# Performance work log

Hardware: AMD Instinct MI355X
Metric: run time of the kernel (lower is better)

The kernel has to match this reference:

```python
import jax, jax.numpy as jnp
import numpy as np

EPS = 1e-6


def setup_inputs() -> dict:
    key = jax.random.key(0)
    k_x, k_w1, k_w2 = jax.random.split(key, 3)
    S, B, H, F = 2048, 4, 2048, 8192
    x = jax.random.normal(k_x, (S, B, H), dtype=jnp.float32)
    scale = jnp.ones((H,), dtype=jnp.float32)
    ln_bias = jnp.zeros((H,), dtype=jnp.float32)
    # kernel_1: [hidden, n_activations=2, intermediate] (GEGLU-style gated MLP)
    kernel_1 = jax.random.normal(k_w1, (H, 2, F), dtype=jnp.float32) * 0.02
    kernel_2 = jax.random.normal(k_w2, (F, H), dtype=jnp.float32) * 0.02
    return {"x": x, "scale": scale, "ln_bias": ln_bias,
            "kernel_1": kernel_1, "kernel_2": kernel_2}


def _layernorm(x, scale, bias):
    # fp32 layernorm over the last (hidden) axis, zero_centered_gamma=False
    mu = jnp.mean(x, axis=-1, keepdims=True)
    var = jnp.mean(jnp.square(x - mu), axis=-1, keepdims=True)
    y = (x - mu) * jax.lax.rsqrt(var + EPS)
    return y * scale + bias


def reference(x, scale, ln_bias, kernel_1, kernel_2):
    # x: [S, B, H] (transpose_batch_sequence=True layout)
    ln_out = _layernorm(x, scale, ln_bias)
    # First GEMM: one projection per activation slice -> [S, B, 2, F]
    z = jnp.einsum("sbh,haf->sbaf", ln_out, kernel_1)
    # activations = ('gelu', 'linear'): gated product
    act = jax.nn.gelu(z[..., 0, :], approximate=True) * z[..., 1, :]
    # Second GEMM: [S, B, F] @ [F, H] -> [S, B, H]
    out = jnp.einsum("sbf,fh->sbh", act, kernel_2)
    return out
```

## Files before the change

kernel.cpp:

```cpp
#include <hip/hip_runtime.h>
#include <hip/hip_bf16.h>

typedef short bf16x8 __attribute__((ext_vector_type(8)));
typedef float f32x4 __attribute__((ext_vector_type(4)));

__device__ inline short f2bf(float f) {
    __bf16 h = (__bf16)f;
    return __builtin_bit_cast(short, h);
}

__device__ inline void gload_lds16(const void* g, void* l) {
    __builtin_amdgcn_global_load_lds(
        (const __attribute__((address_space(1))) void*)g,
        (__attribute__((address_space(3))) void*)l, 16, 0, 0);
}

__global__ __launch_bounds__(256) void ln_kernel(const float* __restrict__ x,
                                                 const float* __restrict__ sc,
                                                 const float* __restrict__ bs,
                                                 short* __restrict__ o) {
    __shared__ float red[8];
    const int row = blockIdx.x;
    const int t = threadIdx.x;
    const float* xr = x + (size_t)row * 2048 + t * 8;
    float4 a = *(const float4*)xr;
    float4 b = *(const float4*)(xr + 4);
    float v[8] = {a.x, a.y, a.z, a.w, b.x, b.y, b.z, b.w};
    float s = 0.f, q = 0.f;
#pragma unroll
    for (int j = 0; j < 8; ++j) { s += v[j]; q += v[j] * v[j]; }
#pragma unroll
    for (int off = 32; off; off >>= 1) {
        s += __shfl_down(s, off, 64);
        q += __shfl_down(q, off, 64);
    }
    const int wv = t >> 6, ln = t & 63;
    if (ln == 0) { red[wv] = s; red[4 + wv] = q; }
    __syncthreads();
    s = red[0] + red[1] + red[2] + red[3];
    q = red[4] + red[5] + red[6] + red[7];
    const float mu = s * (1.f / 2048.f);
    const float var = q * (1.f / 2048.f) - mu * mu;
    const float rstd = rsqrtf(var + 1e-6f);
    const float* scp = sc + t * 8;
    const float* bp = bs + t * 8;
    bf16x8 ov;
#pragma unroll
    for (int j = 0; j < 8; ++j) ov[j] = f2bf((v[j] - mu) * rstd * scp[j] + bp[j]);
    *(bf16x8*)(o + (size_t)row * 2048 + t * 8) = ov;
}

__global__ __launch_bounds__(256) void transpose_conv(const float* __restrict__ src,
                                                      short* __restrict__ dst,
                                                      int R, int C) {
    __shared__ float tile[32][33];
    const int tc = blockIdx.x, tr = blockIdx.y;
    const int t = threadIdx.x;
    const int c = t & 31, r8 = t >> 5;
#pragma unroll
    for (int rr = r8; rr < 32; rr += 8)
        tile[rr][c] = src[(size_t)(tr * 32 + rr) * C + tc * 32 + c];
    __syncthreads();
#pragma unroll
    for (int rr = r8; rr < 32; rr += 8)
        dst[(size_t)(tc * 32 + rr) * R + tr * 32 + c] = f2bf(tile[c][rr]);
}

__global__ __launch_bounds__(256) void gemm1_geglu(const short* __restrict__ A,
                                                   const short* __restrict__ Bt,
                                                   short* __restrict__ act) {
    constexpr int K = 2048;
    constexpr int NACT = 8192;
    __shared__ short As[128 * 32];
    __shared__ short Bs[128 * 32];
    const int t = threadIdx.x;
    const int lane = t & 63;
    const int wv = t >> 6;
    const int wr = wv >> 1, wc = wv & 1;
    const int lr = lane & 15, lg = lane >> 4;
    const int m0 = blockIdx.y * 128;
    const int c0 = blockIdx.x * 64;

    const int srow = t >> 2;
    const int scol = (t & 3) * 8;
    const size_t a_b0 = (size_t)(m0 + srow) * K + scol;
    const size_t a_b1 = (size_t)(m0 + 64 + srow) * K + scol;
    const size_t b_b0 = (size_t)(c0 + srow) * K + scol;
    const size_t b_b1 = (size_t)(8192 + c0 + srow) * K + scol;
    char* asl = (char*)As + t * 16;
    char* bsl = (char*)Bs + t * 16;

    f32x4 acc0[4][2] = {};
    f32x4 acc1[4][2] = {};

    for (int k0 = 0; k0 < K; k0 += 32) {
        __syncthreads();
        gload_lds16(A + a_b0 + k0, asl);
        gload_lds16(A + a_b1 + k0, asl + 4096);
        gload_lds16(Bt + b_b0 + k0, bsl);
        gload_lds16(Bt + b_b1 + k0, bsl + 4096);
        __syncthreads();
        bf16x8 af[4];
#pragma unroll
        for (int m = 0; m < 4; ++m)
            af[m] = *(const bf16x8*)(As + (wr * 64 + m * 16 + lr) * 32 + lg * 8);
        bf16x8 b0[2], b1[2];
#pragma unroll
        for (int n = 0; n < 2; ++n) {
            b0[n] = *(const bf16x8*)(Bs + (wc * 32 + n * 16 + lr) * 32 + lg * 8);
            b1[n] = *(const bf16x8*)(Bs + (64 + wc * 32 + n * 16 + lr) * 32 + lg * 8);
        }
#pragma unroll
        for (int m = 0; m < 4; ++m)
#pragma unroll
            for (int n = 0; n < 2; ++n) {
                acc0[m][n] = __builtin_amdgcn_mfma_f32_16x16x32_bf16(af[m], b0[n], acc0[m][n], 0, 0, 0);
                acc1[m][n] = __builtin_amdgcn_mfma_f32_16x16x32_bf16(af[m], b1[n], acc1[m][n], 0, 0, 0);
            }
    }
#pragma unroll
    for (int m = 0; m < 4; ++m)
#pragma unroll
        for (int n = 0; n < 2; ++n) {
            f32x4 g = acc0[m][n], li = acc1[m][n];
            const int col = c0 + wc * 32 + n * 16 + lr;
            const int rowb = m0 + wr * 64 + m * 16 + lg * 4;
#pragma unroll
            for (int r = 0; r < 4; ++r) {
                float z0 = g[r];
                float ge = 0.5f * z0 * (1.f + tanhf(0.7978845608028654f * (z0 + 0.044715f * z0 * z0 * z0)));
                act[(size_t)(rowb + r) * NACT + col] = f2bf(ge * li[r]);
            }
        }
}

__global__ __launch_bounds__(256) void gemm2(const short* __restrict__ A,
                                             const short* __restrict__ Bt,
                                             float* __restrict__ out) {
    constexpr int K = 8192;
    constexpr int N = 2048;
    __shared__ short As[128 * 32];
    __shared__ short Bs[128 * 32];
    const int t = threadIdx.x;
    const int lane = t & 63;
    const int wv = t >> 6;
    const int wr = wv >> 1, wc = wv & 1;
    const int lr = lane & 15, lg = lane >> 4;
    const int m0 = blockIdx.y * 128;
    const int n0 = blockIdx.x * 128;

    const int srow = t >> 2;
    const int scol = (t & 3) * 8;
    const size_t a_b0 = (size_t)(m0 + srow) * K + scol;
    const size_t a_b1 = (size_t)(m0 + 64 + srow) * K + scol;
    const size_t b_b0 = (size_t)(n0 + srow) * K + scol;
    const size_t b_b1 = (size_t)(n0 + 64 + srow) * K + scol;
    char* asl = (char*)As + t * 16;
    char* bsl = (char*)Bs + t * 16;

    f32x4 acc[4][4] = {};

    for (int k0 = 0; k0 < K; k0 += 32) {
        __syncthreads();
        gload_lds16(A + a_b0 + k0, asl);
        gload_lds16(A + a_b1 + k0, asl + 4096);
        gload_lds16(Bt + b_b0 + k0, bsl);
        gload_lds16(Bt + b_b1 + k0, bsl + 4096);
        __syncthreads();
        bf16x8 af[4], bf[4];
#pragma unroll
        for (int m = 0; m < 4; ++m)
            af[m] = *(const bf16x8*)(As + (wr * 64 + m * 16 + lr) * 32 + lg * 8);
#pragma unroll
        for (int n = 0; n < 4; ++n)
            bf[n] = *(const bf16x8*)(Bs + (wc * 64 + n * 16 + lr) * 32 + lg * 8);
#pragma unroll
        for (int m = 0; m < 4; ++m)
#pragma unroll
            for (int n = 0; n < 4; ++n)
                acc[m][n] = __builtin_amdgcn_mfma_f32_16x16x32_bf16(af[m], bf[n], acc[m][n], 0, 0, 0);
    }
#pragma unroll
    for (int m = 0; m < 4; ++m)
#pragma unroll
        for (int n = 0; n < 4; ++n) {
            const int col = n0 + wc * 64 + n * 16 + lr;
            const int rowb = m0 + wr * 64 + m * 16 + lg * 4;
#pragma unroll
            for (int r = 0; r < 4; ++r)
                out[(size_t)(rowb + r) * N + col] = acc[m][n][r];
        }
}

extern "C" void kernel_launch(void* const* d_in, const int* in_sizes, int n_in,
                              void* d_out, int out_size, void* d_ws, size_t ws_size,
                              hipStream_t stream) {
    const float* x = (const float*)d_in[0];
    const float* scale = (const float*)d_in[1];
    const float* lnb = (const float*)d_in[2];
    const float* w1 = (const float*)d_in[3];
    const float* w2 = (const float*)d_in[4];
    float* out = (float*)d_out;

    const size_t NEED = 268435456;
    if (ws_size < NEED) return;
    char* ws = (char*)d_ws;
    short* lnq = (short*)ws;
    short* w1t = (short*)(ws + 33554432ull);
    short* w2t = (short*)(ws + 100663296ull);
    short* act = (short*)(ws + 134217728ull);

    ln_kernel<<<8192, 256, 0, stream>>>(x, scale, lnb, lnq);
    transpose_conv<<<dim3(512, 64), 256, 0, stream>>>(w1, w1t, 2048, 16384);
    transpose_conv<<<dim3(64, 256), 256, 0, stream>>>(w2, w2t, 8192, 2048);
    gemm1_geglu<<<dim3(128, 64), 256, 0, stream>>>(lnq, w1t, act);
    gemm2<<<dim3(16, 64), 256, 0, stream>>>(act, w2t, out);
}
```

Before: 1.373 ms.

## Rewrite both GEMMs with 256x256 tiles and a four-stage LDS pipeline

Replaces the 128x128 single-buffered GEMM kernels with a shared 512-thread core using 256x256 tiles. It prefetches four K-stages into 128KB of dynamic LDS via global_load_lds, with vmcnt-controlled waits, split barrier phases and raised MFMA priority. The w1 transpose now interleaves gate and linear rows in groups of 16, so each wave holds matching gate and linear accumulators for the GEGLU epilogue. Block IDs are swizzled for L2 locality, and tanh is replaced with an exp-based form. The risks are high register pressure from 32 accumulators per thread and whether this large dynamic LDS allocation launches without an explicit attribute.

```diff
diff --git a/kernel.cpp b/kernel.cpp
--- a/kernel.cpp
+++ b/kernel.cpp
@@ -14,6 +14,9 @@
         (const __attribute__((address_space(1))) void*)g,
         (__attribute__((address_space(3))) void*)l, 16, 0, 0);
 }
+
+#define VMCNT(n) asm volatile("s_waitcnt vmcnt(" #n ")" ::: "memory")
+#define LGK0     asm volatile("s_waitcnt lgkmcnt(0)" ::: "memory")
 
 __global__ __launch_bounds__(256) void ln_kernel(const float* __restrict__ x,
                                                  const float* __restrict__ sc,
@@ -66,130 +69,159 @@
         dst[(size_t)(tc * 32 + rr) * R + tr * 32 + c] = f2bf(tile[c][rr]);
 }
 
-__global__ __launch_bounds__(256) void gemm1_geglu(const short* __restrict__ A,
-                                                   const short* __restrict__ Bt,
-                                                   short* __restrict__ act) {
-    constexpr int K = 2048;
-    constexpr int NACT = 8192;
-    __shared__ short As[128 * 32];
-    __shared__ short Bs[128 * 32];
+__global__ __launch_bounds__(256) void transpose_w1(const float* __restrict__ src,
+                                                    short* __restrict__ dst) {
+    __shared__ float tile[32][33];
+    const int f0 = blockIdx.x * 32;
+    const int k0 = blockIdx.y * 32;
+    const int a = blockIdx.z;
     const int t = threadIdx.x;
-    const int lane = t & 63;
-    const int wv = t >> 6;
-    const int wr = wv >> 1, wc = wv & 1;
+    const int c = t & 31, r8 = t >> 5;
+#pragma unroll
+    for (int rr = r8; rr < 32; rr += 8)
+        tile[rr][c] = src[(size_t)(k0 + rr) * 16384 + a * 8192 + f0 + c];
+    __syncthreads();
+#pragma unroll
+    for (int rr = r8; rr < 32; rr += 8) {
+        const int j = f0 * 2 + (rr & 16) * 2 + a * 16 + (rr & 15);
+        dst[(size_t)j * 2048 + k0 + c] = f2bf(tile[c][rr]);
+    }
+}
+
+template <int K, int NT>
+__device__ inline void gemm_core(const short* __restrict__ A, const short* __restrict__ B,
+                                 int m0, int n0, char* lds, f32x4 (&acc)[8][4]) {
+    const int tid = threadIdx.x;
+    const int lane = tid & 63;
+    const int wid = tid >> 6;
+    const int wr = wid >> 2, wc = wid & 3;
     const int lr = lane & 15, lg = lane >> 4;
-    const int m0 = blockIdx.y * 128;
-    const int c0 = blockIdx.x * 64;
-
-    const int srow = t >> 2;
-    const int scol = (t & 3) * 8;
-    const size_t a_b0 = (size_t)(m0 + srow) * K + scol;
-    const size_t a_b1 = (size_t)(m0 + 64 + srow) * K + scol;
-    const size_t b_b0 = (size_t)(c0 + srow) * K + scol;
-    const size_t b_b1 = (size_t)(8192 + c0 + srow) * K + scol;
-    char* asl = (char*)As + t * 16;
-    char* bsl = (char*)Bs + t * 16;
-
-    f32x4 acc0[4][2] = {};
-    f32x4 acc1[4][2] = {};
-
-    for (int k0 = 0; k0 < K; k0 += 32) {
-        __syncthreads();
-        gload_lds16(A + a_b0 + k0, asl);
-        gload_lds16(A + a_b1 + k0, asl + 4096);
-        gload_lds16(Bt + b_b0 + k0, bsl);
-        gload_lds16(Bt + b_b1 + k0, bsl + 4096);
-        __syncthreads();
-        bf16x8 af[4];
-#pragma unroll
-        for (int m = 0; m < 4; ++m)
-            af[m] = *(const bf16x8*)(As + (wr * 64 + m * 16 + lr) * 32 + lg * 8);
-        bf16x8 b0[2], b1[2];
-#pragma unroll
-        for (int n = 0; n < 2; ++n) {
-            b0[n] = *(const bf16x8*)(Bs + (wc * 32 + n * 16 + lr) * 32 + lg * 8);
-            b1[n] = *(const bf16x8*)(Bs + (64 + wc * 32 + n * 16 + lr) * 32 + lg * 8);
+
+    const short* gA = A + (size_t)(m0 + (tid >> 2)) * K + (tid & 3) * 8;
+    const short* gB = B + (size_t)(n0 + (tid >> 2)) * K + (tid & 3) * 8;
+    char* dA = lds + tid * 16;
+    char* dB = lds + 16384 + tid * 16;
+
+    auto issue = [&](int c) {
+        const int cc = c < 2 * NT - 1 ? c : 2 * NT - 1;
+        const int so = (cc & 3) * 32768;
+        const size_t ko = (size_t)cc * 32;
+        gload_lds16(gA + ko, dA + so);
+        gload_lds16(gA + (size_t)128 * K + ko, dA + so + 8192);
+        gload_lds16(gB + ko, dB + so);
+        gload_lds16(gB + (size_t)128 * K + ko, dB + so + 8192);
+    };
+
+    const int rdA = (wr * 128 + lr) * 64 + lg * 16;
+    const int rdB = 16384 + (wc * 64 + lr) * 64 + lg * 16;
+
+    issue(0); issue(1); issue(2);
+    VMCNT(4);
+    __builtin_amdgcn_s_barrier();
+
+    bf16x8 aF[4], bF[4];
+
+#define PHASE(SB, MH, PRE_ISSUE, PRE_BAR2)                                          \
+    {                                                                               \
+        if ((MH) == 0) {                                                            \
+            _Pragma("unroll") for (int n = 0; n < 4; ++n)                           \
+                bF[n] = *(const bf16x8*)(lds + (SB) + rdB + n * 1024);              \
+        }                                                                           \
+        _Pragma("unroll") for (int m = 0; m < 4; ++m)                               \
+            aF[m] = *(const bf16x8*)(lds + (SB) + rdA + ((MH)*4 + m) * 1024);       \
+        PRE_ISSUE;                                                                  \
+        __builtin_amdgcn_s_barrier();                                               \
+        LGK0;                                                                       \
+        __builtin_amdgcn_s_setprio(1);                                              \
+        _Pragma("unroll") for (int m = 0; m < 4; ++m) {                             \
+            _Pragma("unroll") for (int n = 0; n < 4; ++n)                           \
+                acc[(MH)*4 + m][n] = __builtin_amdgcn_mfma_f32_16x16x32_bf16(       \
+                    aF[m], bF[n], acc[(MH)*4 + m][n], 0, 0, 0);                     \
+        }                                                                           \
+        __builtin_amdgcn_s_setprio(0);                                              \
+        PRE_BAR2;                                                                   \
+        __builtin_amdgcn_s_barrier();                                               \
+    }
+
+#pragma unroll 1
+    for (int tt = 0; tt < NT / 2; ++tt) {
+        const int c0 = 4 * tt;
+        PHASE(0,     0, issue(c0 + 3), (void)0);
+        PHASE(0,     1, (void)0,       (void)0);
+        PHASE(32768, 0, issue(c0 + 4), (void)0);
+        PHASE(32768, 1, (void)0,       VMCNT(4));
+        PHASE(65536, 0, issue(c0 + 5), (void)0);
+        PHASE(65536, 1, (void)0,       (void)0);
+        PHASE(98304, 0, issue(c0 + 6), (void)0);
+        PHASE(98304, 1, (void)0,       VMCNT(4));
+    }
+#undef PHASE
+}
+
+__device__ inline float gelu_tanh(float z) {
+    const float u = 0.7978845608028654f * (z + 0.044715f * z * z * z);
+    const float e = __expf(fminf(2.f * u, 80.f));
+    return 0.5f * z * (1.f + (e - 1.f) / (e + 1.f));
+}
+
+__global__ __launch_bounds__(512, 2) void gemm1_geglu(const short* __restrict__ A,
+                                                      const short* __restrict__ Bt,
+                                                      short* __restrict__ act) {
+    extern __shared__ char lds[];
+    const int bid = blockIdx.x;
+    const int sid = (bid & 7) * 256 + (bid >> 3);
+    const int mb = sid & 31, nb = sid >> 5;
+
+    f32x4 acc[8][4] = {};
+    gemm_core<2048, 32>(A, Bt, mb * 256, nb * 256, lds, acc);
+
+    const int tid = threadIdx.x;
+    const int lane = tid & 63;
+    const int wid = tid >> 6;
+    const int wr = wid >> 2, wc = wid & 3;
+    const int lr = lane & 15, lg = lane >> 4;
+#pragma unroll
+    for (int m = 0; m < 8; ++m) {
+#pragma unroll
+        for (int p = 0; p < 2; ++p) {
+            const f32x4 g = acc[m][2 * p];
+            const f32x4 li = acc[m][2 * p + 1];
+            const int col = nb * 128 + wc * 32 + p * 16 + lr;
+            const int row0 = mb * 256 + wr * 128 + m * 16 + lg * 4;
+#pragma unroll
+            for (int r = 0; r < 4; ++r)
+                act[(size_t)(row0 + r) * 8192 + col] = f2bf(gelu_tanh(g[r]) * li[r]);
         }
-#pragma unroll
-        for (int m = 0; m < 4; ++m)
-#pragma unroll
-            for (int n = 0; n < 2; ++n) {
-                acc0[m][n] = __builtin_amdgcn_mfma_f32_16x16x32_bf16(af[m], b0[n], acc0[m][n], 0, 0, 0);
-                acc1[m][n] = __builtin_amdgcn_mfma_f32_16x16x32_bf16(af[m], b1[n], acc1[m][n], 0, 0, 0);
-            }
-    }
-#pragma unroll
-    for (int m = 0; m < 4; ++m)
-#pragma unroll
-        for (int n = 0; n < 2; ++n) {
-            f32x4 g = acc0[m][n], li = acc1[m][n];
-            const int col = c0 + wc * 32 + n * 16 + lr;
-            const int rowb = m0 + wr * 64 + m * 16 + lg * 4;
-#pragma unroll
-            for (int r = 0; r < 4; ++r) {
-                float z0 = g[r];
-                float ge = 0.5f * z0 * (1.f + tanhf(0.7978845608028654f * (z0 + 0.044715f * z0 * z0 * z0)));
-                act[(size_t)(rowb + r) * NACT + col] = f2bf(ge * li[r]);
-            }
+    }
+}
+
+__global__ __launch_bounds__(512, 2) void gemm2(const short* __restrict__ A,
+                                                const short* __restrict__ Bt,
+                                                float* __restrict__ out) {
+    extern __shared__ char lds[];
+    const int bid = blockIdx.x;
+    const int sid = (bid & 7) * 32 + (bid >> 3);
+    const int mb = sid & 31, nb = sid >> 5;
+
+    f32x4 acc[8][4] = {};
+    gemm_core<8192, 128>(A, Bt, mb * 256, nb * 256, lds, acc);
+
+    const int tid = threadIdx.x;
+    const int lane = tid & 63;
+    const int wid = tid >> 6;
+    const int wr = wid >> 2, wc = wid & 3;
+    const int lr = lane & 15, lg = lane >> 4;
+#pragma unroll
+    for (int m = 0; m < 8; ++m) {
+#pragma unroll
+        for (int n = 0; n < 4; ++n) {
+            const int col = nb * 256 + wc * 64 + n * 16 + lr;
+            const int row0 = mb * 256 + wr * 128 + m * 16 + lg * 4;
+#pragma unroll
+            for (int r = 0; r < 4; ++r)
+                out[(size_t)(row0 + r) * 2048 + col] = acc[m][n][r];
         }
-}
-
-__global__ __launch_bounds__(256) void gemm2(const short* __restrict__ A,
-                                             const short* __restrict__ Bt,
-                                             float* __restrict__ out) {
-    constexpr int K = 8192;
-    constexpr int N = 2048;
-    __shared__ short As[128 * 32];
-    __shared__ short Bs[128 * 32];
-    const int t = threadIdx.x;
-    const int lane = t & 63;
-    const int wv = t >> 6;
-    const int wr = wv >> 1, wc = wv & 1;
-    const int lr = lane & 15, lg = lane >> 4;
-    const int m0 = blockIdx.y * 128;
-    const int n0 = blockIdx.x * 128;
-
-    const int srow = t >> 2;
-    const int scol = (t & 3) * 8;
-    const size_t a_b0 = (size_t)(m0 + srow) * K + scol;
-    const size_t a_b1 = (size_t)(m0 + 64 + srow) * K + scol;
-    const size_t b_b0 = (size_t)(n0 + srow) * K + scol;
-    const size_t b_b1 = (size_t)(n0 + 64 + srow) * K + scol;
-    char* asl = (char*)As + t * 16;
-    char* bsl = (char*)Bs + t * 16;
-
-    f32x4 acc[4][4] = {};
-
-    for (int k0 = 0; k0 < K; k0 += 32) {
-        __syncthreads();
-        gload_lds16(A + a_b0 + k0, asl);
-        gload_lds16(A + a_b1 + k0, asl + 4096);
-        gload_lds16(Bt + b_b0 + k0, bsl);
-        gload_lds16(Bt + b_b1 + k0, bsl + 4096);
-        __syncthreads();
-        bf16x8 af[4], bf[4];
-#pragma unroll
-        for (int m = 0; m < 4; ++m)
-            af[m] = *(const bf16x8*)(As + (wr * 64 + m * 16 + lr) * 32 + lg * 8);
-#pragma unroll
-        for (int n = 0; n < 4; ++n)
-            bf[n] = *(const bf16x8*)(Bs + (wc * 64 + n * 16 + lr) * 32 + lg * 8);
-#pragma unroll
-        for (int m = 0; m < 4; ++m)
-#pragma unroll
-            for (int n = 0; n < 4; ++n)
-                acc[m][n] = __builtin_amdgcn_mfma_f32_16x16x32_bf16(af[m], bf[n], acc[m][n], 0, 0, 0);
-    }
-#pragma unroll
-    for (int m = 0; m < 4; ++m)
-#pragma unroll
-        for (int n = 0; n < 4; ++n) {
-            const int col = n0 + wc * 64 + n * 16 + lr;
-            const int rowb = m0 + wr * 64 + m * 16 + lg * 4;
-#pragma unroll
-            for (int r = 0; r < 4; ++r)
-                out[(size_t)(rowb + r) * N + col] = acc[m][n][r];
-        }
+    }
 }
 
 extern "C" void kernel_launch(void* const* d_in, const int* in_sizes, int n_in,
@@ -211,8 +243,8 @@
     short* act = (short*)(ws + 134217728ull);
 
     ln_kernel<<<8192, 256, 0, stream>>>(x, scale, lnb, lnq);
-    transpose_conv<<<dim3(512, 64), 256, 0, stream>>>(w1, w1t, 2048, 16384);
+    transpose_w1<<<dim3(256, 64, 2), 256, 0, stream>>>(w1, w1t);
     transpose_conv<<<dim3(64, 256), 256, 0, stream>>>(w2, w2t, 8192, 2048);
-    gemm1_geglu<<<dim3(128, 64), 256, 0, stream>>>(lnq, w1t, act);
-    gemm2<<<dim3(16, 64), 256, 0, stream>>>(act, w2t, out);
-}
+    gemm1_geglu<<<2048, 512, 131072, stream>>>(lnq, w1t, act);
+    gemm2<<<256, 512, 131072, stream>>>(act, w2t, out);
+}
```

Measured after the change: 1.282 ms. 6.6% less time.
